# Kernel optimization log

Hardware: AMD Instinct MI355X
Metric: run time of the kernel (lower is better)

## Reference

```python
import jax, jax.numpy as jnp
import numpy as np

N = 50000
E = 800000
DIN = 128
DOUT = 128
T = 4  # number of edge types: onset, consecutive, during, rest


def setup_inputs() -> dict:
    key = jax.random.key(0)
    ks = jax.random.split(key, 12)
    s = 1.0 / np.sqrt(DIN)
    inp = {
        "x": jax.random.normal(ks[0], (N, DIN), dtype=jnp.float32),
        "edge_index": jax.random.randint(ks[1], (2, E), 0, N, dtype=jnp.int32),
        "edge_type": jax.random.randint(ks[2], (E,), 0, T, dtype=jnp.int32),
        # stacked per-etype parameters of ResGatedGraphConv
        "Wk": jax.random.uniform(ks[3], (T, DIN, DOUT), jnp.float32, -s, s),
        "bk": jax.random.uniform(ks[4], (T, DOUT), jnp.float32, -s, s),
        "Wq": jax.random.uniform(ks[5], (T, DIN, DOUT), jnp.float32, -s, s),
        "bq": jax.random.uniform(ks[6], (T, DOUT), jnp.float32, -s, s),
        "Wv": jax.random.uniform(ks[7], (T, DIN, DOUT), jnp.float32, -s, s),
        "bv": jax.random.uniform(ks[8], (T, DOUT), jnp.float32, -s, s),
        "Ws": jax.random.uniform(ks[9], (T, DIN, DOUT), jnp.float32, -s, s),
        "b": jax.random.uniform(ks[10], (T, DOUT), jnp.float32, -s, s),
    }
    return inp


def reference(x, edge_index, edge_type, Wk, bk, Wq, bq, Wv, bv, Ws, b):
    # PyG ResGatedGraphConv per edge type t, with edges masked to that type:
    #   out_i = sum_{j->i, type==t} sigmoid(k_i + q_j) * v_j + Ws_t x_i + b_t
    # followed by mean over edge types ('mean' reduction).
    src = edge_index[0]  # j (message source)
    dst = edge_index[1]  # i (message target)
    n = x.shape[0]
    outs = []
    for t in range(T):
        k = x @ Wk[t] + bk[t]  # [N, DOUT]
        q = x @ Wq[t] + bq[t]
        v = x @ Wv[t] + bv[t]
        eta = jax.nn.sigmoid(k[dst] + q[src])        # [E, DOUT]
        msg = eta * v[src]                            # [E, DOUT]
        msg = jnp.where((edge_type == t)[:, None], msg, 0.0)
        agg = jax.ops.segment_sum(msg, dst, num_segments=n)
        outs.append(agg + x @ Ws[t] + b[t])
    return jnp.mean(jnp.stack(outs, axis=0), axis=0)  # [N, DOUT]
```

## Files before the change

kernel.cpp:

```cpp
#include <hip/hip_runtime.h>

typedef unsigned short u16;
typedef unsigned int u32;
typedef __attribute__((ext_vector_type(8))) short bf16x8;
typedef __attribute__((ext_vector_type(4))) float f32x4;
typedef __attribute__((ext_vector_type(2))) float f32x2;
typedef __attribute__((ext_vector_type(8))) u16 u16x8;
typedef __attribute__((ext_vector_type(4))) u16 u16x4;
typedef __attribute__((ext_vector_type(2))) u16 u16x2;
typedef __attribute__((ext_vector_type(2))) u32 u32x2;

#define DIM 128
#define AS1C(p) ((const __attribute__((address_space(1))) void*)(p))
#define AS3P(p) ((__attribute__((address_space(3))) void*)(p))

__device__ __forceinline__ u32 f2bf(float f){
  u32 x = __float_as_uint(f);
  return (x + 0x7fffu + ((x >> 16) & 1u)) >> 16;
}
__device__ __forceinline__ float bf2f(u16 u){
  return __uint_as_float(((u32)u) << 16);
}

__global__ __launch_bounds__(256) void prep_kernel(
    const float* __restrict__ x, u16* __restrict__ xb,
    const float* __restrict__ Wk, const float* __restrict__ bk,
    const float* __restrict__ Wq, const float* __restrict__ bq,
    const float* __restrict__ Wv, const float* __restrict__ bv,
    const float* __restrict__ Ws, const float* __restrict__ bb,
    u16* __restrict__ WcatT, float* __restrict__ biascat,
    int* __restrict__ cnt, int T, int N, int rows){
  int id = blockIdx.x * 256 + threadIdx.x;
  int total_w = (3 * T + 1) * DIM * DIM;
  int total_cast = rows * (DIM / 4);
  if (id >= total_w){
    int z = id - total_w;
    if (z < total_cast){
      int el = z * 4;
      int node = el >> 7;
      u32x2 pk;
      if (node < N){
        f32x4 v = *(const f32x4*)(x + el);
        pk.x = f2bf(v.x) | (f2bf(v.y) << 16);
        pk.y = f2bf(v.z) | (f2bf(v.w) << 16);
      } else { pk.x = 0u; pk.y = 0u; }
      *(u32x2*)(xb + el) = pk;
    } else {
      int z2 = z - total_cast;
      if (z2 < N) cnt[z2] = 0;
    }
    return;
  }
  int kk = id & (DIM - 1);
  int c  = id >> 7;
  int qvspan = 2 * T * DIM;
  float wv, bvv;
  if (c < qvspan){
    int t = c >> 8;
    int w = c & 255;
    int j = w >> 1;
    if ((w & 1) == 0){ wv = Wq[(t*DIM + kk)*DIM + j]; bvv = bq[t*DIM + j]; }
    else             { wv = Wv[(t*DIM + kk)*DIM + j]; bvv = bv[t*DIM + j]; }
  } else if (c < qvspan + T * DIM){
    int t = (c - qvspan) >> 7;
    int j = (c - qvspan) & (DIM - 1);
    wv = Wk[(t*DIM + kk)*DIM + j]; bvv = bk[t*DIM + j];
  } else {
    int j = c - 3 * T * DIM;
    float s = 0.f, sb = 0.f;
    for (int t = 0; t < T; ++t){ s += Ws[(t*DIM + kk)*DIM + j]; sb += bb[t*DIM + j]; }
    wv = s / (float)T; bvv = sb / (float)T;
  }
  WcatT[(size_t)c * DIM + kk] = (u16)f2bf(wv);
  if (kk == 0) biascat[c] = bvv;
}

__global__ __launch_bounds__(256) void hist_kernel(const int* __restrict__ dst,
                                                   int* __restrict__ cnt,
                                                   int* __restrict__ rank, int E){
  int e = blockIdx.x * 256 + threadIdx.x;
  if (e < E) rank[e] = atomicAdd(&cnt[dst[e]], 1);
}

__global__ __launch_bounds__(256) void scan1_kernel(const int* __restrict__ cnt,
                                                    int* __restrict__ offs,
                                                    int* __restrict__ bsum, int n){
  __shared__ int wsum[4];
  const int tid = threadIdx.x;
  const int lane = tid & 63, wave = tid >> 6;
  const int base = blockIdx.x * 2048 + tid * 8;
  int v[8]; int tot = 0;
#pragma unroll
  for (int j = 0; j < 8; ++j){
    int idx = base + j;
    int val = (idx < n) ? cnt[idx] : 0;
    v[j] = val; tot += val;
  }
  int incl = tot;
#pragma unroll
  for (int d = 1; d < 64; d <<= 1){
    int u = __shfl_up(incl, d, 64);
    if (lane >= d) incl += u;
  }
  if (lane == 63) wsum[wave] = incl;
  __syncthreads();
  int wbase = 0;
#pragma unroll
  for (int w = 0; w < 4; ++w) if (w < wave) wbase += wsum[w];
  int excl = wbase + incl - tot;
  if (tid == 255) bsum[blockIdx.x] = wbase + incl;
#pragma unroll
  for (int j = 0; j < 8; ++j){
    int idx = base + j;
    if (idx < n) offs[idx] = excl;
    excl += v[j];
  }
}

__global__ __launch_bounds__(64) void scan2_kernel(const int* __restrict__ bsum,
                                                   int* __restrict__ boffs, int nb){
  int lane = threadIdx.x;
  int v = (lane < nb) ? bsum[lane] : 0;
  int incl = v;
#pragma unroll
  for (int d = 1; d < 64; d <<= 1){
    int u = __shfl_up(incl, d, 64);
    if (lane >= d) incl += u;
  }
  if (lane < nb) boffs[lane] = incl - v;
}

__global__ __launch_bounds__(256) void scatter_kernel(const int* __restrict__ src,
                                                      const int* __restrict__ dst,
                                                      const int* __restrict__ et,
                                                      const int* __restrict__ offs,
                                                      const int* __restrict__ boffs,
                                                      const int* __restrict__ rank,
                                                      int* __restrict__ packed, int E){
  int e = blockIdx.x * 256 + threadIdx.x;
  if (e >= E) return;
  int d = dst[e];
  int pos = offs[d] + boffs[d >> 11] + rank[e];
  packed[pos] = (src[e] << 2) | (et[e] & 3);
}

__global__ __launch_bounds__(256, 2) void gemm_kernel(const u16* __restrict__ xb,
                                                      const u16* __restrict__ WcatT,
                                                      const float* __restrict__ biascat,
                                                      u16* __restrict__ Y,
                                                      int N, int ncol){
  __shared__ u16 xt[DIM * DIM];
  __shared__ u16 wt[DIM * DIM];
  const int n0 = blockIdx.x * 128;
  const int m0 = blockIdx.y * 128;
  const int tid  = threadIdx.x;
  const int wave = tid >> 6;
  const int lane = tid & 63;
  const int l15  = lane & 15;
  const int quad = lane >> 4;
  const int wrow = wave * 32;

#pragma unroll
  for (int it = 0; it < 8; ++it){
    int s  = it * 256 + tid;
    int r  = s >> 4;
    int p  = s & 15;
    int lb = p ^ (r & 7);
    int lbase = (it * 256 + wave * 64) * 8;
    __builtin_amdgcn_global_load_lds(AS1C(xb + (size_t)(m0 + r) * DIM + lb * 8),
                                     AS3P(xt + lbase), 16, 0, 0);
    __builtin_amdgcn_global_load_lds(AS1C(WcatT + (size_t)(n0 + r) * DIM + lb * 8),
                                     AS3P(wt + lbase), 16, 0, 0);
  }
  __syncthreads();

  f32x4 acc[2][8];
#pragma unroll
  for (int mt = 0; mt < 2; ++mt)
#pragma unroll
    for (int nt = 0; nt < 8; ++nt)
      acc[mt][nt] = (f32x4){0.f, 0.f, 0.f, 0.f};

#pragma unroll
  for (int ks = 0; ks < 4; ++ks){
    const int pb8 = (((ks * 4 + quad) ^ (l15 & 7)) * 8);
    bf16x8 bfr[2], afr[8];
#pragma unroll
    for (int mt = 0; mt < 2; ++mt)
      bfr[mt] = *(const bf16x8*)&xt[(wrow + mt * 16 + l15) * DIM + pb8];
#pragma unroll
    for (int f = 0; f < 8; ++f)
      afr[f] = *(const bf16x8*)&wt[(f * 16 + l15) * DIM + pb8];
#pragma unroll
    for (int f = 0; f < 8; ++f)
#pragma unroll
      for (int mt = 0; mt < 2; ++mt)
        acc[mt][f] = __builtin_amdgcn_mfma_f32_16x16x32_bf16(afr[f], bfr[mt], acc[mt][f], 0, 0, 0);
  }

#pragma unroll
  for (int mt = 0; mt < 2; ++mt){
    int node = m0 + wrow + mt * 16 + l15;
    if (node >= N) continue;
    size_t rowbase = (size_t)node * ncol;
#pragma unroll
    for (int f = 0; f < 8; ++f){
      int feat = n0 + f * 16 + quad * 4;
      f32x4 b4 = *(const f32x4*)&biascat[feat];
      f32x4 v  = acc[mt][f];
      u32 lo = f2bf(v.x + b4.x) | (f2bf(v.y + b4.y) << 16);
      u32 hi = f2bf(v.z + b4.z) | (f2bf(v.w + b4.w) << 16);
      u32x2 pk = {lo, hi};
      *(u32x2*)&Y[rowbase + feat] = pk;
    }
  }
}

__global__ __launch_bounds__(256) void agg_kernel(const u16* __restrict__ Y,
                                                  const int* __restrict__ offs,
                                                  const int* __restrict__ boffs,
                                                  const int* __restrict__ packed,
                                                  float* __restrict__ out,
                                                  int N, int E, float invT, int ncol){
  const int wave = threadIdx.x >> 6;
  const int lane = threadIdx.x & 63;
  const int half = lane >> 5;
  const int l32  = lane & 31;
  const int node = blockIdx.x * 8 + wave * 2 + half;
  const bool valid = node < N;
  const int nc = valid ? node : N - 1;

  const int kqoff = 1024;
  const int soff  = 1536;
  const u16* yr = Y + (size_t)nc * ncol;
  const int c4 = l32 * 4;

  u16x4 kw[4];
#pragma unroll
  for (int t = 0; t < 4; ++t)
    kw[t] = *(const u16x4*)(yr + kqoff + t * DIM + c4);
  u16x4 sw = *(const u16x4*)(yr + soff + c4);

  int e0 = 0, e1 = 0;
  if (valid){
    e0 = offs[nc] + boffs[nc >> 11];
    e1 = (nc == N - 1) ? E : (offs[nc + 1] + boffs[(nc + 1) >> 11]);
  }

  f32x4 acc = {0.f, 0.f, 0.f, 0.f};
  int e = e0;
  for (; e + 4 <= e1; e += 4){
    int p[4];
#pragma unroll
    for (int j = 0; j < 4; ++j) p[j] = packed[e + j];
    u16x8 a[4];
#pragma unroll
    for (int j = 0; j < 4; ++j)
      a[j] = *(const u16x8*)(Y + (size_t)(p[j] >> 2) * ncol + (p[j] & 3) * 256 + l32 * 8);
#pragma unroll
    for (int j = 0; j < 4; ++j){
      int t = p[j] & 3;
      u16x4 kwt = (t == 0) ? kw[0] : (t == 1) ? kw[1] : (t == 2) ? kw[2] : kw[3];
      acc.x += bf2f(a[j].s1) * __builtin_amdgcn_rcpf(1.f + __expf(-(bf2f(kwt.x) + bf2f(a[j].s0))));
      acc.y += bf2f(a[j].s3) * __builtin_amdgcn_rcpf(1.f + __expf(-(bf2f(kwt.y) + bf2f(a[j].s2))));
      acc.z += bf2f(a[j].s5) * __builtin_amdgcn_rcpf(1.f + __expf(-(bf2f(kwt.z) + bf2f(a[j].s4))));
      acc.w += bf2f(a[j].s7) * __builtin_amdgcn_rcpf(1.f + __expf(-(bf2f(kwt.w) + bf2f(a[j].s6))));
    }
  }
  for (; e < e1; ++e){
    int p = packed[e];
    int t = p & 3;
    u16x8 a = *(const u16x8*)(Y + (size_t)(p >> 2) * ncol + t * 256 + l32 * 8);
    u16x4 kwt = (t == 0) ? kw[0] : (t == 1) ? kw[1] : (t == 2) ? kw[2] : kw[3];
    acc.x += bf2f(a.s1) * __builtin_amdgcn_rcpf(1.f + __expf(-(bf2f(kwt.x) + bf2f(a.s0))));
    acc.y += bf2f(a.s3) * __builtin_amdgcn_rcpf(1.f + __expf(-(bf2f(kwt.y) + bf2f(a.s2))));
    acc.z += bf2f(a.s5) * __builtin_amdgcn_rcpf(1.f + __expf(-(bf2f(kwt.z) + bf2f(a.s4))));
    acc.w += bf2f(a.s7) * __builtin_amdgcn_rcpf(1.f + __expf(-(bf2f(kwt.w) + bf2f(a.s6))));
  }
  if (valid){
    f32x4 o = { invT * acc.x + bf2f(sw.x), invT * acc.y + bf2f(sw.y),
                invT * acc.z + bf2f(sw.z), invT * acc.w + bf2f(sw.w) };
    *(f32x4*)&out[(size_t)node * DIM + c4] = o;
  }
}

extern "C" void kernel_launch(void* const* d_in, const int* in_sizes, int n_in,
                              void* d_out, int out_size, void* d_ws, size_t ws_size,
                              hipStream_t stream){
  const float* x  = (const float*)d_in[0];
  const int*   ei = (const int*)d_in[1];
  const int*   et = (const int*)d_in[2];
  const float* Wk = (const float*)d_in[3];
  const float* bk = (const float*)d_in[4];
  const float* Wq = (const float*)d_in[5];
  const float* bq = (const float*)d_in[6];
  const float* Wv = (const float*)d_in[7];
  const float* bv = (const float*)d_in[8];
  const float* Ws = (const float*)d_in[9];
  const float* bb = (const float*)d_in[10];
  float* out = (float*)d_out;

  const int N = in_sizes[0] / DIM;
  const int E = in_sizes[2];
  const int T = in_sizes[3] / (DIM * DIM);
  const int NB = 3 * T + 1;
  const int ncol = NB * DIM;
  const int mtiles = (N + 127) / 128;
  const int rows = mtiles * 128;
  const int nscan = (N + 2047) / 2048;

  char* ws = (char*)d_ws;
  size_t off = 0;
  auto alloc = [&](size_t bytes) -> char* {
    char* p = ws + off;
    off = (off + bytes + 255) & ~(size_t)255;
    return p;
  };
  u16*   xb      = (u16*)alloc((size_t)rows * DIM * 2);
  u16*   WcatT   = (u16*)alloc((size_t)ncol * DIM * 2);
  float* biascat = (float*)alloc((size_t)ncol * 4);
  u16*   Y       = (u16*)alloc((size_t)N * ncol * 2);
  int*   cnt     = (int*)alloc((size_t)N * 4);
  int*   offs    = (int*)alloc((size_t)N * 4);
  int*   rank    = (int*)alloc((size_t)E * 4);
  int*   packed  = (int*)alloc((size_t)E * 4);
  int*   bsum    = (int*)alloc((size_t)nscan * 4);
  int*   boffs   = (int*)alloc((size_t)nscan * 4);
  (void)ws_size; (void)n_in; (void)out_size;

  const int* srcp = ei;
  const int* dstp = ei + E;

  int prep_total = NB * DIM * DIM + rows * (DIM / 4) + N;
  prep_kernel<<<(prep_total + 255) / 256, 256, 0, stream>>>(x, xb, Wk, bk, Wq, bq, Wv, bv,
                                                            Ws, bb, WcatT, biascat, cnt, T, N, rows);
  hist_kernel<<<(E + 255) / 256, 256, 0, stream>>>(dstp, cnt, rank, E);
  scan1_kernel<<<nscan, 256, 0, stream>>>(cnt, offs, bsum, N);
  scan2_kernel<<<1, 64, 0, stream>>>(bsum, boffs, nscan);
  scatter_kernel<<<(E + 255) / 256, 256, 0, stream>>>(srcp, dstp, et, offs, boffs, rank, packed, E);
  dim3 g(NB, mtiles);
  gemm_kernel<<<g, 256, 0, stream>>>(xb, WcatT, biascat, Y, N, ncol);
  agg_kernel<<<(N + 7) / 8, 256, 0, stream>>>(Y, offs, boffs, packed, out, N, E, 1.0f / (float)T, ncol);
}
```

Before: 309.7 us.

## Stream x fragments from global in GEMM, remap tiles, deepen aggregation unroll

The GEMM no longer stages x tiles in LDS. Each wave loads its own x rows straight into registers, prefetching one k-step ahead, which halves shared memory and allows four blocks per CU. Blocks are remapped into groups of eight m-tiles sharing an n-tile to improve L2 reuse of weights. The aggregation loop is unrolled from four to eight edges per iteration to keep more gathers in flight, at the cost of more registers.

```diff
diff --git a/kernel.cpp b/kernel.cpp
--- a/kernel.cpp
+++ b/kernel.cpp
@@ -144,15 +144,27 @@
   packed[pos] = (src[e] << 2) | (et[e] & 3);
 }
 
-__global__ __launch_bounds__(256, 2) void gemm_kernel(const u16* __restrict__ xb,
+__global__ __launch_bounds__(256, 4) void gemm_kernel(const u16* __restrict__ xb,
                                                       const u16* __restrict__ WcatT,
                                                       const float* __restrict__ biascat,
                                                       u16* __restrict__ Y,
-                                                      int N, int ncol){
-  __shared__ u16 xt[DIM * DIM];
+                                                      int N, int ncol, int NB, int mtiles){
   __shared__ u16 wt[DIM * DIM];
-  const int n0 = blockIdx.x * 128;
-  const int m0 = blockIdx.y * 128;
+  int bid = blockIdx.x;
+  int body = NB * (mtiles & ~7);
+  int mt, nt;
+  if (bid < body){
+    int g = bid >> 3, r = bid & 7;
+    int a = g / NB;
+    mt = a * 8 + r;
+    nt = g - a * NB;
+  } else {
+    int z = bid - body;
+    mt = (mtiles & ~7) + z / NB;
+    nt = z % NB;
+  }
+  const int m0 = mt * 128;
+  const int n0 = nt * 128;
   const int tid  = threadIdx.x;
   const int wave = tid >> 6;
   const int lane = tid & 63;
@@ -160,6 +172,15 @@
   const int quad = lane >> 4;
   const int wrow = wave * 32;
 
+  const u16* xrow0 = xb + (size_t)(m0 + wrow + l15) * DIM + quad * 8;
+  const u16* xrow1 = xrow0 + 16 * DIM;
+
+  bf16x8 bcur[2], bnxt[2];
+  bcur[0] = *(const bf16x8*)(xrow0 + 0);
+  bcur[1] = *(const bf16x8*)(xrow1 + 0);
+  bnxt[0] = *(const bf16x8*)(xrow0 + 32);
+  bnxt[1] = *(const bf16x8*)(xrow1 + 32);
+
 #pragma unroll
   for (int it = 0; it < 8; ++it){
     int s  = it * 256 + tid;
@@ -167,8 +188,6 @@
     int p  = s & 15;
     int lb = p ^ (r & 7);
     int lbase = (it * 256 + wave * 64) * 8;
-    __builtin_amdgcn_global_load_lds(AS1C(xb + (size_t)(m0 + r) * DIM + lb * 8),
-                                     AS3P(xt + lbase), 16, 0, 0);
     __builtin_amdgcn_global_load_lds(AS1C(WcatT + (size_t)(n0 + r) * DIM + lb * 8),
                                      AS3P(wt + lbase), 16, 0, 0);
   }
@@ -176,38 +195,40 @@
 
   f32x4 acc[2][8];
 #pragma unroll
-  for (int mt = 0; mt < 2; ++mt)
-#pragma unroll
-    for (int nt = 0; nt < 8; ++nt)
-      acc[mt][nt] = (f32x4){0.f, 0.f, 0.f, 0.f};
+  for (int m = 0; m < 2; ++m)
+#pragma unroll
+    for (int f = 0; f < 8; ++f)
+      acc[m][f] = (f32x4){0.f, 0.f, 0.f, 0.f};
 
 #pragma unroll
   for (int ks = 0; ks < 4; ++ks){
+    bf16x8 b0 = bcur[0], b1 = bcur[1];
+    if (ks < 3){
+      bcur[0] = bnxt[0]; bcur[1] = bnxt[1];
+      if (ks < 2){
+        bnxt[0] = *(const bf16x8*)(xrow0 + (ks + 2) * 32);
+        bnxt[1] = *(const bf16x8*)(xrow1 + (ks + 2) * 32);
+      }
+    }
     const int pb8 = (((ks * 4 + quad) ^ (l15 & 7)) * 8);
-    bf16x8 bfr[2], afr[8];
-#pragma unroll
-    for (int mt = 0; mt < 2; ++mt)
-      bfr[mt] = *(const bf16x8*)&xt[(wrow + mt * 16 + l15) * DIM + pb8];
-#pragma unroll
-    for (int f = 0; f < 8; ++f)
-      afr[f] = *(const bf16x8*)&wt[(f * 16 + l15) * DIM + pb8];
-#pragma unroll
-    for (int f = 0; f < 8; ++f)
-#pragma unroll
-      for (int mt = 0; mt < 2; ++mt)
-        acc[mt][f] = __builtin_amdgcn_mfma_f32_16x16x32_bf16(afr[f], bfr[mt], acc[mt][f], 0, 0, 0);
-  }
-
-#pragma unroll
-  for (int mt = 0; mt < 2; ++mt){
-    int node = m0 + wrow + mt * 16 + l15;
+#pragma unroll
+    for (int f = 0; f < 8; ++f){
+      bf16x8 afr = *(const bf16x8*)&wt[(f * 16 + l15) * DIM + pb8];
+      acc[0][f] = __builtin_amdgcn_mfma_f32_16x16x32_bf16(afr, b0, acc[0][f], 0, 0, 0);
+      acc[1][f] = __builtin_amdgcn_mfma_f32_16x16x32_bf16(afr, b1, acc[1][f], 0, 0, 0);
+    }
+  }
+
+#pragma unroll
+  for (int m = 0; m < 2; ++m){
+    int node = m0 + wrow + m * 16 + l15;
     if (node >= N) continue;
     size_t rowbase = (size_t)node * ncol;
 #pragma unroll
     for (int f = 0; f < 8; ++f){
       int feat = n0 + f * 16 + quad * 4;
       f32x4 b4 = *(const f32x4*)&biascat[feat];
-      f32x4 v  = acc[mt][f];
+      f32x4 v  = acc[m][f];
       u32 lo = f2bf(v.x + b4.x) | (f2bf(v.y + b4.y) << 16);
       u32 hi = f2bf(v.z + b4.z) | (f2bf(v.w + b4.w) << 16);
       u32x2 pk = {lo, hi};
@@ -249,16 +270,16 @@
 
   f32x4 acc = {0.f, 0.f, 0.f, 0.f};
   int e = e0;
-  for (; e + 4 <= e1; e += 4){
-    int p[4];
-#pragma unroll
-    for (int j = 0; j < 4; ++j) p[j] = packed[e + j];
-    u16x8 a[4];
-#pragma unroll
-    for (int j = 0; j < 4; ++j)
+  for (; e + 8 <= e1; e += 8){
+    int p[8];
+#pragma unroll
+    for (int j = 0; j < 8; ++j) p[j] = packed[e + j];
+    u16x8 a[8];
+#pragma unroll
+    for (int j = 0; j < 8; ++j)
       a[j] = *(const u16x8*)(Y + (size_t)(p[j] >> 2) * ncol + (p[j] & 3) * 256 + l32 * 8);
 #pragma unroll
-    for (int j = 0; j < 4; ++j){
+    for (int j = 0; j < 8; ++j){
       int t = p[j] & 3;
       u16x4 kwt = (t == 0) ? kw[0] : (t == 1) ? kw[1] : (t == 2) ? kw[2] : kw[3];
       acc.x += bf2f(a[j].s1) * __builtin_amdgcn_rcpf(1.f + __expf(-(bf2f(kwt.x) + bf2f(a[j].s0))));
@@ -338,7 +359,6 @@
   scan1_kernel<<<nscan, 256, 0, stream>>>(cnt, offs, bsum, N);
   scan2_kernel<<<1, 64, 0, stream>>>(bsum, boffs, nscan);
   scatter_kernel<<<(E + 255) / 256, 256, 0, stream>>>(srcp, dstp, et, offs, boffs, rank, packed, E);
-  dim3 g(NB, mtiles);
-  gemm_kernel<<<g, 256, 0, stream>>>(xb, WcatT, biascat, Y, N, ncol);
+  gemm_kernel<<<NB * mtiles, 256, 0, stream>>>(xb, WcatT, biascat, Y, N, ncol, NB, mtiles);
   agg_kernel<<<(N + 7) / 8, 256, 0, stream>>>(Y, offs, boffs, packed, out, N, E, 1.0f / (float)T, ncol);
 }
```

Result: no change. 306.1 us (-1.2%).
